# Performance work log

Hardware: AMD Instinct MI355X
Metric: run time of the kernel (lower is better)

The kernel has to match this reference:

```python
import jax, jax.numpy as jnp
import numpy as np

N = 4096
VOCAB = 50257
EDIM = 1024
WFEAT = 1024
LABELS = 2
SLOPE = 0.01
NEG_INF = -1e9


def setup_inputs() -> dict:
    key = jax.random.key(0)
    ks = jax.random.split(key, 8)
    inSen = jax.random.randint(ks[0], (N,), 0, VOCAB, dtype=jnp.int64)
    adj = jax.random.randint(ks[1], (N, N), 0, 2, dtype=jnp.int32)
    emb_table = jax.random.normal(ks[2], (VOCAB, EDIM), dtype=jnp.float32) * 0.02
    W = jax.random.normal(ks[3], (EDIM, WFEAT), dtype=jnp.float32) * (1.0 / np.sqrt(EDIM))
    a_src = jax.random.normal(ks[4], (WFEAT,), dtype=jnp.float32) * (1.0 / np.sqrt(WFEAT))
    a_dst = jax.random.normal(ks[5], (WFEAT,), dtype=jnp.float32) * (1.0 / np.sqrt(WFEAT))
    clf_w = jax.random.normal(ks[6], (WFEAT, LABELS), dtype=jnp.float32) * (1.0 / np.sqrt(WFEAT))
    clf_b = jax.random.normal(ks[7], (LABELS,), dtype=jnp.float32) * 0.01
    return {"inSen": inSen, "adj": adj, "emb_table": emb_table, "W": W,
            "a_src": a_src, "a_dst": a_dst, "clf_w": clf_w, "clf_b": clf_b}


def reference(inSen, adj, emb_table, W, a_src, a_dst, clf_w, clf_b):
    # Embedding lookup: [N, edim]
    words = emb_table[inSen]
    # GAT layer: linear projection [N, wFeat]
    h = words @ W
    # Pairwise attention logits e_ij = LeakyReLU(a_src.h_i + a_dst.h_j)
    s_src = h @ a_src            # [N]
    s_dst = h @ a_dst            # [N]
    e = jax.nn.leaky_relu(s_src[:, None] + s_dst[None, :], negative_slope=SLOPE)  # [N, N]
    # Adjacency-masked softmax over neighbors (axis=1)
    e = jnp.where(adj > 0, e, NEG_INF)
    attention = jax.nn.softmax(e, axis=1)          # [N, N]
    sentence = attention @ h                       # [N, wFeat]
    # Mean pooling over nodes
    poolSentence = jnp.mean(sentence, axis=0)      # [wFeat]
    # Classifier + softmax over labels (dim=0 of a 1-D vector)
    label = jax.nn.softmax(poolSentence @ clf_w + clf_b, axis=0)  # [labels]
    return (poolSentence, attention, sentence, label)
```

## Files before the change

### kernel.cpp

```cpp
#include <hip/hip_runtime.h>
#include <hip/hip_bf16.h>

#define NN 4096
#define ED 1024
#define WF 1024
#define SLOPEC 0.01f
#define NEG_INFC -1e9f

typedef __attribute__((ext_vector_type(8))) short bf16x8;
typedef __attribute__((ext_vector_type(4))) short short4v;
typedef __attribute__((ext_vector_type(4))) float f32x4;

__device__ __forceinline__ float bf2f(short s) {
    union { unsigned u; float f; } v;
    v.u = ((unsigned)(unsigned short)s) << 16;
    return v.f;
}
__device__ __forceinline__ short f2bf(float f) {
    unsigned u = __float_as_uint(f);
    unsigned r = u + 0x7FFFu + ((u >> 16) & 1u);
    return (short)(r >> 16);
}

typedef __attribute__((address_space(3))) unsigned lds_u32;
typedef const __attribute__((address_space(1))) unsigned gbl_u32;
__device__ __forceinline__ void g2l16(const short* g, short* l) {
    __builtin_amdgcn_global_load_lds((gbl_u32*)g, (lds_u32*)l, 16, 0, 0);
}

__global__ __launch_bounds__(256) void k_wt(const float* __restrict__ W,
                                            short* __restrict__ Wt) {
    __shared__ float t[64][65];
    const int k0 = blockIdx.y * 64, n0 = blockIdx.x * 64;
    const int tx = threadIdx.x & 63, ty = threadIdx.x >> 6;
#pragma unroll
    for (int p = 0; p < 16; p++) {
        int r = p * 4 + ty;
        t[r][tx] = W[(long)(k0 + r) * WF + n0 + tx];
    }
    __syncthreads();
#pragma unroll
    for (int p = 0; p < 16; p++) {
        int r = p * 4 + ty;
        Wt[(long)(n0 + r) * ED + k0 + tx] = f2bf(t[tx][r]);
    }
}

__global__ __launch_bounds__(256) void k_gather(const int* __restrict__ inSen,
                                                const float* __restrict__ emb,
                                                short* __restrict__ X) {
    const int row = blockIdx.x;
    const int tid = threadIdx.x;
    const long idx = inSen[row];
    const float4 v = ((const float4*)(emb + idx * ED))[tid];
    short4v s;
    s.x = f2bf(v.x); s.y = f2bf(v.y); s.z = f2bf(v.z); s.w = f2bf(v.w);
    *(short4v*)(X + (long)row * ED + tid * 4) = s;
}

template <int BM, int BN, bool BF16_OUT>
__global__ __launch_bounds__(256, 2) void gemm_bt2(
    const short* __restrict__ A, const short* __restrict__ Bt,
    int M, int N, int K, int Kc, void* __restrict__ Cout, long MN) {
    constexpr int TM = BM / 32;
    constexpr int TN = BN / 32;
    constexpr int STAGE = BM * 32 + BN * 32;
    constexpr int SMEMSZ = (BF16_OUT && BM * BN > STAGE) ? BM * BN : STAGE;
    __shared__ __align__(16) short smem[SMEMSZ];
    short* sA = smem;
    short* sB = smem + BM * 32;

    const int tid = threadIdx.x;
    const int lane = tid & 63;
    const int wid = tid >> 6;
    const int wm = wid >> 1, wn = wid & 1;
    const int n0 = blockIdx.x * BN;
    const int m0 = blockIdx.y * BM;
    const int ks = blockIdx.z * Kc;

    const int srow = tid >> 2;
    const int sc8 = (tid & 3) * 8;
    const int l15 = lane & 15;
    const int lhi = lane >> 4;

    f32x4 acc[TM][TN];
#pragma unroll
    for (int t = 0; t < TM; t++)
#pragma unroll
        for (int u = 0; u < TN; u++) acc[t][u] = (f32x4){0.f, 0.f, 0.f, 0.f};

    const short* Ab = A + (long)(m0 + srow) * K + ks + sc8;
    const short* Bb = Bt + (long)(n0 + srow) * K + ks + sc8;
    const long rstep = (long)64 * K;

    for (int k0 = 0; k0 < Kc; k0 += 32) {
#pragma unroll
        for (int p = 0; p < BM / 64; p++)
            g2l16(Ab + p * rstep + k0, sA + (p * 256 + wid * 64) * 8);
#pragma unroll
        for (int p = 0; p < BN / 64; p++)
            g2l16(Bb + p * rstep + k0, sB + (p * 256 + wid * 64) * 8);
        __syncthreads();

        bf16x8 af[TM], bfr[TN];
#pragma unroll
        for (int t = 0; t < TM; t++)
            af[t] = *(const bf16x8*)&sA[(wm * (BM / 2) + t * 16 + l15) * 32 + lhi * 8];
#pragma unroll
        for (int u = 0; u < TN; u++)
            bfr[u] = *(const bf16x8*)&sB[(wn * (BN / 2) + u * 16 + l15) * 32 + lhi * 8];
#pragma unroll
        for (int t = 0; t < TM; t++)
#pragma unroll
            for (int u = 0; u < TN; u++)
                acc[t][u] = __builtin_amdgcn_mfma_f32_16x16x32_bf16(
                    af[t], bfr[u], acc[t][u], 0, 0, 0);
        __syncthreads();
    }

    if (BF16_OUT) {
        short* sT = smem;
#pragma unroll
        for (int t = 0; t < TM; t++)
#pragma unroll
            for (int u = 0; u < TN; u++)
#pragma unroll
                for (int r = 0; r < 4; r++) {
                    int m = wm * (BM / 2) + t * 16 + lhi * 4 + r;
                    int n = wn * (BN / 2) + u * 16 + l15;
                    sT[m * BN + n] = f2bf(acc[t][u][r]);
                }
        __syncthreads();
        short* C = (short*)Cout;
#pragma unroll
        for (int q = 0; q < BM * BN / 2048; q++) {
            int idx = q * 256 + tid;
            int row = idx / (BN / 8);
            int c8 = (idx % (BN / 8)) * 8;
            *(bf16x8*)(C + (long)(m0 + row) * N + n0 + c8) =
                *(const bf16x8*)&sT[row * BN + c8];
        }
    } else {
        float* P = (float*)Cout + (long)blockIdx.z * MN;
#pragma unroll
        for (int t = 0; t < TM; t++)
#pragma unroll
            for (int u = 0; u < TN; u++)
#pragma unroll
                for (int r = 0; r < 4; r++) {
                    int m = wm * (BM / 2) + t * 16 + lhi * 4 + r;
                    int n = wn * (BN / 2) + u * 16 + l15;
                    P[(long)(m0 + m) * N + n0 + n] = acc[t][u][r];
                }
    }
}

__global__ __launch_bounds__(256) void k_scores(const short* __restrict__ Ht,
                                                const float* __restrict__ a_src,
                                                const float* __restrict__ a_dst,
                                                float* __restrict__ s_src,
                                                float* __restrict__ s_dst) {
    const int i = blockIdx.x * 256 + threadIdx.x;
    const int f0 = blockIdx.y * 256;
    float as = 0.f, ad = 0.f;
#pragma unroll 8
    for (int f = f0; f < f0 + 256; f++) {
        float hv = bf2f(Ht[(long)f * NN + i]);
        as += hv * a_src[f];
        ad += hv * a_dst[f];
    }
    atomicAdd(s_src + i, as);
    atomicAdd(s_dst + i, ad);
}

__global__ __launch_bounds__(256) void k_attn(const int* __restrict__ adj,
                                              const float* __restrict__ s_src,
                                              const float* __restrict__ s_dst,
                                              float* __restrict__ attn,
                                              short* __restrict__ attnB) {
    __shared__ float wred[4];
    __shared__ float wred2[4];
    const int row = blockIdx.x;
    const int tid = threadIdx.x;
    const float ss = s_src[row];
    const int4* adj4 = (const int4*)(adj + (long)row * NN);
    const float4* sd4 = (const float4*)s_dst;
    float v[16];
    float vmax = -3e38f;
#pragma unroll
    for (int c = 0; c < 4; c++) {
        int idx = c * 256 + tid;
        int4 a = adj4[idx];
        float4 d = sd4[idx];
        float x0 = ss + d.x; x0 = x0 > 0.f ? x0 : SLOPEC * x0; x0 = a.x > 0 ? x0 : NEG_INFC;
        float x1 = ss + d.y; x1 = x1 > 0.f ? x1 : SLOPEC * x1; x1 = a.y > 0 ? x1 : NEG_INFC;
        float x2 = ss + d.z; x2 = x2 > 0.f ? x2 : SLOPEC * x2; x2 = a.z > 0 ? x2 : NEG_INFC;
        float x3 = ss + d.w; x3 = x3 > 0.f ? x3 : SLOPEC * x3; x3 = a.w > 0 ? x3 : NEG_INFC;
        v[c * 4 + 0] = x0; v[c * 4 + 1] = x1; v[c * 4 + 2] = x2; v[c * 4 + 3] = x3;
        vmax = fmaxf(vmax, fmaxf(fmaxf(x0, x1), fmaxf(x2, x3)));
    }
#pragma unroll
    for (int off = 32; off; off >>= 1) vmax = fmaxf(vmax, __shfl_xor(vmax, off));
    if ((tid & 63) == 0) wred[tid >> 6] = vmax;
    __syncthreads();
    vmax = fmaxf(fmaxf(wred[0], wred[1]), fmaxf(wred[2], wred[3]));

    float sum = 0.f;
#pragma unroll
    for (int c = 0; c < 16; c++) {
        v[c] = __expf(v[c] - vmax);
        sum += v[c];
    }
#pragma unroll
    for (int off = 32; off; off >>= 1) sum += __shfl_xor(sum, off);
    if ((tid & 63) == 0) wred2[tid >> 6] = sum;
    __syncthreads();
    sum = wred2[0] + wred2[1] + wred2[2] + wred2[3];
    const float inv = 1.0f / sum;

    float4* o4 = (float4*)(attn + (long)row * NN);
    short4v* b4 = (short4v*)(attnB + (long)row * NN);
#pragma unroll
    for (int c = 0; c < 4; c++) {
        int idx = c * 256 + tid;
        float4 o;
        o.x = v[c * 4 + 0] * inv; o.y = v[c * 4 + 1] * inv;
        o.z = v[c * 4 + 2] * inv; o.w = v[c * 4 + 3] * inv;
        o4[idx] = o;
        short4v sb;
        sb.x = f2bf(o.x); sb.y = f2bf(o.y); sb.z = f2bf(o.z); sb.w = f2bf(o.w);
        b4[idx] = sb;
    }
}

__global__ __launch_bounds__(256) void k_reduce2(const float* __restrict__ P,
                                                 float* __restrict__ sent,
                                                 float* __restrict__ pool) {
    const int tid = threadIdx.x;
    const long MN4 = (long)NN * WF / 4;
    const float4* P0 = (const float4*)P;
    const float4* P1 = P0 + MN4;
    float4* s4 = (float4*)sent;
    float4 acc = {0.f, 0.f, 0.f, 0.f};
#pragma unroll 4
    for (int r = 0; r < 16; r++) {
        long e = (long)(blockIdx.x * 16 + r) * 256 + tid;
        float4 a = P0[e], b = P1[e];
        float4 s;
        s.x = a.x + b.x; s.y = a.y + b.y; s.z = a.z + b.z; s.w = a.w + b.w;
        s4[e] = s;
        acc.x += s.x; acc.y += s.y; acc.z += s.z; acc.w += s.w;
    }
    atomicAdd(pool + tid * 4 + 0, acc.x);
    atomicAdd(pool + tid * 4 + 1, acc.y);
    atomicAdd(pool + tid * 4 + 2, acc.z);
    atomicAdd(pool + tid * 4 + 3, acc.w);
}

__global__ __launch_bounds__(256) void k_final(const float* __restrict__ pool_acc,
                                               const float* __restrict__ clf_w,
                                               const float* __restrict__ clf_b,
                                               float* __restrict__ out_pool,
                                               float* __restrict__ out_label) {
    __shared__ float r0[4], r1[4];
    const int tid = threadIdx.x;
    float l0 = 0.f, l1 = 0.f;
#pragma unroll
    for (int q = 0; q < 4; q++) {
        int f = q * 256 + tid;
        float p = pool_acc[f] * (1.0f / NN);
        out_pool[f] = p;
        l0 += p * clf_w[f * 2 + 0];
        l1 += p * clf_w[f * 2 + 1];
    }
#pragma unroll
    for (int off = 32; off; off >>= 1) {
        l0 += __shfl_xor(l0, off);
        l1 += __shfl_xor(l1, off);
    }
    if ((tid & 63) == 0) { r0[tid >> 6] = l0; r1[tid >> 6] = l1; }
    __syncthreads();
    if (tid == 0) {
        float L0 = r0[0] + r0[1] + r0[2] + r0[3] + clf_b[0];
        float L1 = r1[0] + r1[1] + r1[2] + r1[3] + clf_b[1];
        float m = fmaxf(L0, L1);
        float e0 = __expf(L0 - m), e1 = __expf(L1 - m);
        float s = e0 + e1;
        out_label[0] = e0 / s;
        out_label[1] = e1 / s;
    }
}

extern "C" void kernel_launch(void* const* d_in, const int* in_sizes, int n_in,
                              void* d_out, int out_size, void* d_ws,
                              size_t ws_size, hipStream_t stream) {
    const int* inSen = (const int*)d_in[0];
    const int* adj = (const int*)d_in[1];
    const float* emb = (const float*)d_in[2];
    const float* W = (const float*)d_in[3];
    const float* a_src = (const float*)d_in[4];
    const float* a_dst = (const float*)d_in[5];
    const float* clf_w = (const float*)d_in[6];
    const float* clf_b = (const float*)d_in[7];

    float* out = (float*)d_out;
    float* out_pool = out;
    float* attn = out + 1024;
    float* sentence = out + 1024 + (long)NN * NN;
    float* out_label = out + 1024 + (long)NN * NN + (long)NN * WF;

    char* ws = (char*)d_ws;
    short* X = (short*)ws;
    short* Wt = (short*)(ws + (8l << 20));
    short* Ht = (short*)(ws + (10l << 20));
    short* attnB = (short*)(ws + (18l << 20));
    float* P2 = (float*)(ws + (52l << 20));
    float* s_src = (float*)(ws + (86l << 20));
    float* s_dst = s_src + NN;
    float* pool = s_dst + NN;

    hipMemsetAsync(s_src, 0, (2 * NN + WF) * sizeof(float), stream);

    k_wt<<<dim3(16, 16), 256, 0, stream>>>(W, Wt);
    k_gather<<<NN, 256, 0, stream>>>(inSen, emb, X);

    gemm_bt2<64, 128, true><<<dim3(NN / 128, WF / 64, 1), 256, 0, stream>>>(
        Wt, X, WF, NN, ED, ED, Ht, 0);

    k_scores<<<dim3(NN / 256, WF / 256), 256, 0, stream>>>(Ht, a_src, a_dst,
                                                           s_src, s_dst);
    k_attn<<<NN, 256, 0, stream>>>(adj, s_src, s_dst, attn, attnB);

    gemm_bt2<128, 128, false><<<dim3(WF / 128, NN / 128, 2), 256, 0, stream>>>(
        attnB, Ht, NN, WF, NN, NN / 2, P2, (long)NN * WF);

    k_reduce2<<<NN / 16, 256, 0, stream>>>(P2, sentence, pool);
    k_final<<<1, 256, 0, stream>>>(pool, clf_w, clf_b, out_pool, out_label);
}
```

Measured before the change: 446.5 us.

## Fuse prep kernels, fold score dot-products into GEMM epilogue, split-K by four

Merges the W transpose and embedding gather into one launch. Computes s_src/s_dst inside the first GEMM's epilogue from the fp32 accumulators, which removes the separate strided score kernel. Raises the attention GEMM split-K from 2 to 4 and widens the reduction to sum four partial buffers. Adds nontemporal loads and stores for adj and the fp32 outputs. The larger split-K doubles the partial-buffer traffic in exchange for more blocks in flight, and the epilogue adds atomics per GEMM tile.

Result: faster. 431.9 us (-3.3%).

```diff
diff --git a/kernel.cpp b/kernel.cpp
--- a/kernel.cpp
+++ b/kernel.cpp
@@ -10,6 +10,7 @@
 typedef __attribute__((ext_vector_type(8))) short bf16x8;
 typedef __attribute__((ext_vector_type(4))) short short4v;
 typedef __attribute__((ext_vector_type(4))) float f32x4;
+typedef __attribute__((ext_vector_type(4))) int int4v;
 
 __device__ __forceinline__ float bf2f(short s) {
     union { unsigned u; float f; } v;
@@ -28,40 +29,43 @@
     __builtin_amdgcn_global_load_lds((gbl_u32*)g, (lds_u32*)l, 16, 0, 0);
 }
 
-__global__ __launch_bounds__(256) void k_wt(const float* __restrict__ W,
-                                            short* __restrict__ Wt) {
-    __shared__ float t[64][65];
-    const int k0 = blockIdx.y * 64, n0 = blockIdx.x * 64;
-    const int tx = threadIdx.x & 63, ty = threadIdx.x >> 6;
-#pragma unroll
-    for (int p = 0; p < 16; p++) {
-        int r = p * 4 + ty;
-        t[r][tx] = W[(long)(k0 + r) * WF + n0 + tx];
-    }
-    __syncthreads();
-#pragma unroll
-    for (int p = 0; p < 16; p++) {
-        int r = p * 4 + ty;
-        Wt[(long)(n0 + r) * ED + k0 + tx] = f2bf(t[tx][r]);
-    }
-}
-
-__global__ __launch_bounds__(256) void k_gather(const int* __restrict__ inSen,
-                                                const float* __restrict__ emb,
-                                                short* __restrict__ X) {
-    const int row = blockIdx.x;
-    const int tid = threadIdx.x;
-    const long idx = inSen[row];
-    const float4 v = ((const float4*)(emb + idx * ED))[tid];
-    short4v s;
-    s.x = f2bf(v.x); s.y = f2bf(v.y); s.z = f2bf(v.z); s.w = f2bf(v.w);
-    *(short4v*)(X + (long)row * ED + tid * 4) = s;
-}
-
-template <int BM, int BN, bool BF16_OUT>
+__global__ __launch_bounds__(256) void k_prep(const float* __restrict__ W,
+                                              short* __restrict__ Wt,
+                                              const int* __restrict__ inSen,
+                                              const float* __restrict__ emb,
+                                              short* __restrict__ X) {
+    if (blockIdx.x < 256) {
+        __shared__ float t[64][65];
+        const int n0 = (blockIdx.x & 15) * 64, k0 = (blockIdx.x >> 4) * 64;
+        const int tx = threadIdx.x & 63, ty = threadIdx.x >> 6;
+#pragma unroll
+        for (int p = 0; p < 16; p++) {
+            int r = p * 4 + ty;
+            t[r][tx] = W[(long)(k0 + r) * WF + n0 + tx];
+        }
+        __syncthreads();
+#pragma unroll
+        for (int p = 0; p < 16; p++) {
+            int r = p * 4 + ty;
+            Wt[(long)(n0 + r) * ED + k0 + tx] = f2bf(t[tx][r]);
+        }
+    } else {
+        const int row = blockIdx.x - 256;
+        const int tid = threadIdx.x;
+        const long idx = inSen[row];
+        const float4 v = ((const float4*)(emb + idx * ED))[tid];
+        short4v s;
+        s.x = f2bf(v.x); s.y = f2bf(v.y); s.z = f2bf(v.z); s.w = f2bf(v.w);
+        *(short4v*)(X + (long)row * ED + tid * 4) = s;
+    }
+}
+
+template <int BM, int BN, bool BF16_OUT, bool DO_SCORES>
 __global__ __launch_bounds__(256, 2) void gemm_bt2(
     const short* __restrict__ A, const short* __restrict__ Bt,
-    int M, int N, int K, int Kc, void* __restrict__ Cout, long MN) {
+    int M, int N, int K, int Kc, void* __restrict__ Cout, long MN,
+    const float* __restrict__ a_src, const float* __restrict__ a_dst,
+    float* __restrict__ s_src, float* __restrict__ s_dst) {
     constexpr int TM = BM / 32;
     constexpr int TN = BN / 32;
     constexpr int STAGE = BM * 32 + BN * 32;
@@ -140,6 +144,36 @@
             *(bf16x8*)(C + (long)(m0 + row) * N + n0 + c8) =
                 *(const bf16x8*)&sT[row * BN + c8];
         }
+        if (DO_SCORES) {
+            float ps[TN], pd[TN];
+#pragma unroll
+            for (int u = 0; u < TN; u++) { ps[u] = 0.f; pd[u] = 0.f; }
+#pragma unroll
+            for (int t = 0; t < TM; t++)
+#pragma unroll
+                for (int r = 0; r < 4; r++) {
+                    int m = m0 + wm * (BM / 2) + t * 16 + lhi * 4 + r;
+                    float as = a_src[m], ad = a_dst[m];
+#pragma unroll
+                    for (int u = 0; u < TN; u++) {
+                        ps[u] += acc[t][u][r] * as;
+                        pd[u] += acc[t][u][r] * ad;
+                    }
+                }
+#pragma unroll
+            for (int u = 0; u < TN; u++) {
+                ps[u] += __shfl_xor(ps[u], 16); ps[u] += __shfl_xor(ps[u], 32);
+                pd[u] += __shfl_xor(pd[u], 16); pd[u] += __shfl_xor(pd[u], 32);
+            }
+            if (lane < 16) {
+#pragma unroll
+                for (int u = 0; u < TN; u++) {
+                    int n = n0 + wn * (BN / 2) + u * 16 + lane;
+                    atomicAdd(s_src + n, ps[u]);
+                    atomicAdd(s_dst + n, pd[u]);
+                }
+            }
+        }
     } else {
         float* P = (float*)Cout + (long)blockIdx.z * MN;
 #pragma unroll
@@ -153,24 +187,6 @@
                     P[(long)(m0 + m) * N + n0 + n] = acc[t][u][r];
                 }
     }
-}
-
-__global__ __launch_bounds__(256) void k_scores(const short* __restrict__ Ht,
-                                                const float* __restrict__ a_src,
-                                                const float* __restrict__ a_dst,
-                                                float* __restrict__ s_src,
-                                                float* __restrict__ s_dst) {
-    const int i = blockIdx.x * 256 + threadIdx.x;
-    const int f0 = blockIdx.y * 256;
-    float as = 0.f, ad = 0.f;
-#pragma unroll 8
-    for (int f = f0; f < f0 + 256; f++) {
-        float hv = bf2f(Ht[(long)f * NN + i]);
-        as += hv * a_src[f];
-        ad += hv * a_dst[f];
-    }
-    atomicAdd(s_src + i, as);
-    atomicAdd(s_dst + i, ad);
 }
 
 __global__ __launch_bounds__(256) void k_attn(const int* __restrict__ adj,
@@ -183,15 +199,15 @@
     const int row = blockIdx.x;
     const int tid = threadIdx.x;
     const float ss = s_src[row];
-    const int4* adj4 = (const int4*)(adj + (long)row * NN);
-    const float4* sd4 = (const float4*)s_dst;
+    const int4v* adj4 = (const int4v*)(adj + (long)row * NN);
+    const f32x4* sd4 = (const f32x4*)s_dst;
     float v[16];
     float vmax = -3e38f;
 #pragma unroll
     for (int c = 0; c < 4; c++) {
         int idx = c * 256 + tid;
-        int4 a = adj4[idx];
-        float4 d = sd4[idx];
+        int4v a = __builtin_nontemporal_load(&adj4[idx]);
+        f32x4 d = sd4[idx];
         float x0 = ss + d.x; x0 = x0 > 0.f ? x0 : SLOPEC * x0; x0 = a.x > 0 ? x0 : NEG_INFC;
         float x1 = ss + d.y; x1 = x1 > 0.f ? x1 : SLOPEC * x1; x1 = a.y > 0 ? x1 : NEG_INFC;
         float x2 = ss + d.z; x2 = x2 > 0.f ? x2 : SLOPEC * x2; x2 = a.z > 0 ? x2 : NEG_INFC;
@@ -218,15 +234,15 @@
     sum = wred2[0] + wred2[1] + wred2[2] + wred2[3];
     const float inv = 1.0f / sum;
 
-    float4* o4 = (float4*)(attn + (long)row * NN);
+    f32x4* o4 = (f32x4*)(attn + (long)row * NN);
     short4v* b4 = (short4v*)(attnB + (long)row * NN);
 #pragma unroll
     for (int c = 0; c < 4; c++) {
         int idx = c * 256 + tid;
-        float4 o;
+        f32x4 o;
         o.x = v[c * 4 + 0] * inv; o.y = v[c * 4 + 1] * inv;
         o.z = v[c * 4 + 2] * inv; o.w = v[c * 4 + 3] * inv;
-        o4[idx] = o;
+        __builtin_nontemporal_store(o, &o4[idx]);
         short4v sb;
         sb.x = f2bf(o.x); sb.y = f2bf(o.y); sb.z = f2bf(o.z); sb.w = f2bf(o.w);
         b4[idx] = sb;
@@ -238,18 +254,17 @@
                                                  float* __restrict__ pool) {
     const int tid = threadIdx.x;
     const long MN4 = (long)NN * WF / 4;
-    const float4* P0 = (const float4*)P;
-    const float4* P1 = P0 + MN4;
-    float4* s4 = (float4*)sent;
-    float4 acc = {0.f, 0.f, 0.f, 0.f};
+    const f32x4* P0 = (const f32x4*)P;
+    f32x4* s4 = (f32x4*)sent;
+    f32x4 acc = {0.f, 0.f, 0.f, 0.f};
 #pragma unroll 4
     for (int r = 0; r < 16; r++) {
         long e = (long)(blockIdx.x * 16 + r) * 256 + tid;
-        float4 a = P0[e], b = P1[e];
-        float4 s;
-        s.x = a.x + b.x; s.y = a.y + b.y; s.z = a.z + b.z; s.w = a.w + b.w;
-        s4[e] = s;
-        acc.x += s.x; acc.y += s.y; acc.z += s.z; acc.w += s.w;
+        f32x4 a = P0[e], b = P0[e + MN4];
+        f32x4 c = P0[e + 2 * MN4], d = P0[e + 3 * MN4];
+        f32x4 s = a + b + c + d;
+        __builtin_nontemporal_store(s, &s4[e]);
+        acc += s;
     }
     atomicAdd(pool + tid * 4 + 0, acc.x);
     atomicAdd(pool + tid * 4 + 1, acc.y);
@@ -315,24 +330,22 @@
     short* Ht = (short*)(ws + (10l << 20));
     short* attnB = (short*)(ws + (18l << 20));
     float* P2 = (float*)(ws + (52l << 20));
-    float* s_src = (float*)(ws + (86l << 20));
+    float* s_src = (float*)(ws + (120l << 20));
     float* s_dst = s_src + NN;
     float* pool = s_dst + NN;
 
-    hipMemsetAsync(s_src, 0, (2 * NN + WF) * sizeof(float), stream);
-
-    k_wt<<<dim3(16, 16), 256, 0, stream>>>(W, Wt);
-    k_gather<<<NN, 256, 0, stream>>>(inSen, emb, X);
-
-    gemm_bt2<64, 128, true><<<dim3(NN / 128, WF / 64, 1), 256, 0, stream>>>(
-        Wt, X, WF, NN, ED, ED, Ht, 0);
-
-    k_scores<<<dim3(NN / 256, WF / 256), 256, 0, stream>>>(Ht, a_src, a_dst,
-                                                           s_src, s_dst);
+    (void)hipMemsetAsync(s_src, 0, (2 * NN + WF) * sizeof(float), stream);
+
+    k_prep<<<256 + NN, 256, 0, stream>>>(W, Wt, inSen, emb, X);
+
+    gemm_bt2<64, 128, true, true><<<dim3(NN / 128, WF / 64, 1), 256, 0, stream>>>(
+        Wt, X, WF, NN, ED, ED, Ht, 0, a_src, a_dst, s_src, s_dst);
+
     k_attn<<<NN, 256, 0, stream>>>(adj, s_src, s_dst, attn, attnB);
 
-    gemm_bt2<128, 128, false><<<dim3(WF / 128, NN / 128, 2), 256, 0, stream>>>(
-        attnB, Ht, NN, WF, NN, NN / 2, P2, (long)NN * WF);
+    gemm_bt2<128, 128, false, false><<<dim3(WF / 128, NN / 128, 4), 256, 0, stream>>>(
+        attnB, Ht, NN, WF, NN, NN / 4, P2, (long)NN * WF,
+        nullptr, nullptr, nullptr, nullptr);
 
     k_reduce2<<<NN / 16, 256, 0, stream>>>(P2, sentence, pool);
     k_final<<<1, 256, 0, stream>>>(pool, clf_w, clf_b, out_pool, out_label);
```
